# Kernel tuning notes

Hardware: AMD Instinct MI355X
Metric: run time of the kernel (lower is better)

The kernel has to match this reference:

```python
import jax, jax.numpy as jnp
import numpy as np

N0 = 50000  # nodes of type n0
N1 = 50000  # nodes of type n1
E = 160000  # edges per relation
IN_FEAT = 128
OUT_FEAT = 128
NUM_BASES = 2
NUM_RELS = 4


def setup_inputs() -> dict:
    key = jax.random.key(0)
    ks = jax.random.split(key, 12)
    inp = {
        "x0": jax.random.normal(ks[0], (N0, IN_FEAT), dtype=jnp.float32),
        "x1": jax.random.normal(ks[1], (N1, IN_FEAT), dtype=jnp.float32),
        "weight": jax.random.normal(ks[2], (NUM_BASES, IN_FEAT, OUT_FEAT), dtype=jnp.float32) * 0.05,
        "w_comp": jax.random.normal(ks[3], (NUM_RELS, NUM_BASES), dtype=jnp.float32),
        "h_bias": jnp.zeros((OUT_FEAT,), dtype=jnp.float32),
    }
    # relation i: (src ntype, dst ntype) = (0,0), (0,1), (1,0), (1,1)
    inp["src0"] = jax.random.randint(ks[4], (E,), 0, N0, dtype=jnp.int32)
    inp["dst0"] = jax.random.randint(ks[5], (E,), 0, N0, dtype=jnp.int32)
    inp["src1"] = jax.random.randint(ks[6], (E,), 0, N0, dtype=jnp.int32)
    inp["dst1"] = jax.random.randint(ks[7], (E,), 0, N1, dtype=jnp.int32)
    inp["src2"] = jax.random.randint(ks[8], (E,), 0, N1, dtype=jnp.int32)
    inp["dst2"] = jax.random.randint(ks[9], (E,), 0, N0, dtype=jnp.int32)
    inp["src3"] = jax.random.randint(ks[10], (E,), 0, N1, dtype=jnp.int32)
    inp["dst3"] = jax.random.randint(ks[11], (E,), 0, N1, dtype=jnp.int32)
    return inp


def _rel_msg(x_src, W_r, src, dst, n_dst):
    # per-relation: transform all src features, gather per edge, scatter-sum to dst
    h = x_src @ W_r            # [N_src, out]
    m = jnp.take(h, src, axis=0)  # [E, out]
    return jax.ops.segment_sum(m, dst, num_segments=n_dst)


def reference(x0, x1, weight, w_comp, h_bias,
              src0, dst0, src1, dst1, src2, dst2, src3, dst3):
    # basis regularizer: compose per-relation weights from shared bases
    W = jnp.einsum('rb,bio->rio', w_comp, weight)  # [num_rels, in, out]
    # cross-reducer 'sum': sum aggregated messages per destination node type
    agg0 = _rel_msg(x0, W[0], src0, dst0, N0) + _rel_msg(x1, W[2], src2, dst2, N0)
    agg1 = _rel_msg(x0, W[1], src1, dst1, N1) + _rel_msg(x1, W[3], src3, dst3, N1)
    h0 = agg0 + h_bias  # bias; activation=None, self_loop=False, dropout=0
    h1 = agg1 + h_bias
    return (h0, h1)
```

## Files before the change

### kernel.cpp

```cpp
#include <hip/hip_runtime.h>
#include <hip/hip_bf16.h>

typedef __bf16 bf16x8 __attribute__((ext_vector_type(8)));
typedef float f32x4 __attribute__((ext_vector_type(4)));

#define N_NODES 50000
#define NEDGE 160000
#define NSLOT (2 * N_NODES)
#define NB 3125
#define CAPS 96
#define SCAP 768
#define HSZ ((size_t)N_NODES * 128)
#define FILL_BLKS 2500
#define GEMM_BLKS 1564

constexpr size_t OFF_WFRAG = 0;
constexpr size_t OFF_H     = 131072;
constexpr size_t OFF_CNT   = OFF_H + 4 * 12800000;
constexpr size_t OFF_SBEG  = OFF_CNT + 1600000;
constexpr size_t OFF_SCNT  = OFF_SBEG + 401408;
constexpr size_t OFF_EBUF  = OFF_SCNT + 401408;
constexpr size_t OFF_SRC   = OFF_EBUF + 9600000;

__global__ __launch_bounds__(256) void wfrag_kernel(const float* __restrict__ weight,
                                                    const float* __restrict__ wcomp,
                                                    __bf16* __restrict__ wfrag,
                                                    int* __restrict__ cnt) {
    int tid = blockIdx.x * 256 + threadIdx.x;
    if (tid < NB * 8) cnt[tid * 16] = 0;
    int j    = tid & 7;
    int lane = (tid >> 3) & 63;
    int kk   = (tid >> 9) & 3;
    int n    = (tid >> 11) & 7;
    int r    = tid >> 14;
    int k = kk * 32 + ((lane >> 4) << 3) + j;
    int o = (n << 4) + (lane & 15);
    float v = wcomp[r * 2] * weight[k * 128 + o] +
              wcomp[r * 2 + 1] * weight[16384 + k * 128 + o];
    wfrag[tid] = (__bf16)v;
}

__global__ __launch_bounds__(256) void gemm_fill_kernel(const float* __restrict__ x0,
                                                        const float* __restrict__ x1,
                                                        const __bf16* __restrict__ wfrag,
                                                        __bf16* __restrict__ Hbase,
                                                        const int* __restrict__ s0, const int* __restrict__ d0,
                                                        const int* __restrict__ s1, const int* __restrict__ d1,
                                                        const int* __restrict__ s2, const int* __restrict__ d2,
                                                        const int* __restrict__ s3, const int* __restrict__ d3,
                                                        int* __restrict__ cnt,
                                                        unsigned int* __restrict__ ebuf) {
    __shared__ __bf16 wl[16384];
    int bid = blockIdx.x;

    if (bid < FILL_BLKS) {
        int rel = bid / 625;
        int e = (bid - rel * 625) * 256 + threadIdx.x;
        int sub = bid & 7;
        const int* sp = rel == 0 ? s0 : rel == 1 ? s1 : rel == 2 ? s2 : s3;
        const int* dp = rel == 0 ? d0 : rel == 1 ? d1 : rel == 2 ? d2 : d3;
        int slot = dp[e] + ((rel & 1) ? N_NODES : 0);
        unsigned int w = (unsigned)sp[e] | ((unsigned)(slot & 31) << 16) |
                         ((rel >= 2) ? (1u << 21) : 0u);
        int seg = (slot >> 5) * 8 + sub;
        int pos = atomicAdd(&cnt[seg * 16], 1);
        if (pos < CAPS) ebuf[seg * CAPS + pos] = w;
        return;
    }

    int gid = bid - FILL_BLKS;
    const int y = gid / 782;
    const int xb = gid - y * 782;
    const float* x = y ? x1 : x0;

    const int lane = threadIdx.x & 63;
    const int wave = threadIdx.x >> 6;
    const int g = lane >> 4;
    const int m15 = lane & 15;

    int node = xb * 64 + wave * 16 + m15;
    int rowc = node < N_NODES ? node : N_NODES - 1;
    const float* xr = x + (size_t)rowc * 128 + g * 8;

    bf16x8 a[4];
#pragma unroll
    for (int kk = 0; kk < 4; ++kk) {
        float4 f0 = *reinterpret_cast<const float4*>(xr + kk * 32);
        float4 f1 = *reinterpret_cast<const float4*>(xr + kk * 32 + 4);
        bf16x8 t;
        t[0] = (__bf16)f0.x; t[1] = (__bf16)f0.y; t[2] = (__bf16)f0.z; t[3] = (__bf16)f0.w;
        t[4] = (__bf16)f1.x; t[5] = (__bf16)f1.y; t[6] = (__bf16)f1.z; t[7] = (__bf16)f1.w;
        a[kk] = t;
    }

    const bf16x8* wv = reinterpret_cast<const bf16x8*>(wl);
    bool valid = node < N_NODES;

#pragma unroll
    for (int rr = 0; rr < 2; ++rr) {
        int rel = 2 * y + rr;
        if (rr) __syncthreads();
        {
            const uint4* s = reinterpret_cast<const uint4*>(wfrag + rel * 16384);
            uint4* dsl = reinterpret_cast<uint4*>(wl);
            int t = threadIdx.x;
#pragma unroll
            for (int i = 0; i < 8; ++i) dsl[t + i * 256] = s[t + i * 256];
        }
        __syncthreads();

        __bf16* H = Hbase + (size_t)rel * HSZ;
#pragma unroll
        for (int n = 0; n < 8; ++n) {
            f32x4 acc = (f32x4){0.f, 0.f, 0.f, 0.f};
#pragma unroll
            for (int kk = 0; kk < 4; ++kk)
                acc = __builtin_amdgcn_mfma_f32_16x16x32_bf16(
                    wv[(n * 4 + kk) * 64 + lane], a[kk], acc, 0, 0, 0);
            if (valid) {
                union { __bf16 b[4]; uint2 u; } pk;
                pk.b[0] = (__bf16)acc[0]; pk.b[1] = (__bf16)acc[1];
                pk.b[2] = (__bf16)acc[2]; pk.b[3] = (__bf16)acc[3];
                *reinterpret_cast<uint2*>(&H[(size_t)node * 128 + n * 16 + g * 4]) = pk.u;
            }
        }
    }
}

__global__ __launch_bounds__(256) void bucket_sort_kernel(const unsigned int* __restrict__ ebuf,
                                                          const int* __restrict__ cnt,
                                                          int* __restrict__ srcids,
                                                          int* __restrict__ sbeg,
                                                          unsigned int* __restrict__ scnt) {
    __shared__ int sbuf[SCAP];
    __shared__ int lcnt[64];
    __shared__ int lcur[64];
    __shared__ int stotal;
    int b = blockIdx.x;
    int t = threadIdx.x;
    if (t < 64) lcnt[t] = 0;
    for (int j = t; j < SCAP; j += 256) sbuf[j] = 0;
    __syncthreads();

    int cs[8];
#pragma unroll
    for (int s = 0; s < 8; ++s) {
        int c = cnt[(b * 8 + s) * 16];
        cs[s] = c < CAPS ? c : CAPS;
    }
#pragma unroll
    for (int s = 0; s < 8; ++s)
        for (int j = t; j < cs[s]; j += 256) {
            unsigned int w = ebuf[(b * 8 + s) * CAPS + j];
            int key = ((w >> 15) & 62) | ((w >> 21) & 1);
            atomicAdd(&lcnt[key], 1);
        }
    __syncthreads();

    if (t < 64) {
        int cA = (t < 32) ? lcnt[2 * t] : 0;
        int cB = (t < 32) ? lcnt[2 * t + 1] : 0;
        int pad = (cA + cB + 3) & ~3;
        int s = pad;
#pragma unroll
        for (int dd = 1; dd < 64; dd <<= 1) {
            int n = __shfl_up(s, dd, 64);
            if (t >= dd) s += n;
        }
        int start = s - pad;
        if (t < 32) {
            lcur[2 * t] = start;
            lcur[2 * t + 1] = start + cA;
            sbeg[b * 32 + t] = b * SCAP + start;
            scnt[b * 32 + t] = (unsigned)cA | ((unsigned)cB << 16);
            if (t == 31) stotal = start + pad;
        }
    }
    __syncthreads();

#pragma unroll
    for (int s = 0; s < 8; ++s)
        for (int j = t; j < cs[s]; j += 256) {
            unsigned int w = ebuf[(b * 8 + s) * CAPS + j];
            int key = ((w >> 15) & 62) | ((w >> 21) & 1);
            int pos = atomicAdd(&lcur[key], 1);
            sbuf[pos] = (int)(w & 0xffffu);
        }
    __syncthreads();

    int n = stotal;
    int* du = srcids + (size_t)b * SCAP;
    for (int j = t; j < n; j += 256) du[j] = sbuf[j];
}

__global__ __launch_bounds__(256) void aggregate_all_kernel(const __bf16* __restrict__ Hbase,
                                                            const int* __restrict__ sbeg,
                                                            const unsigned int* __restrict__ scnt,
                                                            const int* __restrict__ srcids,
                                                            const float* __restrict__ bias,
                                                            float* __restrict__ out) {
    int idx = blockIdx.x * 256 + threadIdx.x;
    int slot = idx >> 6;
    int lane = idx & 63;
    int p = slot >= N_NODES;

    int beg = __builtin_amdgcn_readfirstlane(sbeg[slot]);
    unsigned int c = (unsigned int)__builtin_amdgcn_readfirstlane((int)scnt[slot]);
    int dA = (int)(c & 0xffffu);
    int d  = dA + (int)(c >> 16);
    const int* sp = srcids + beg;

    const unsigned int* HA = reinterpret_cast<const unsigned int*>(Hbase + (size_t)p * HSZ);
    const unsigned int* HB = reinterpret_cast<const unsigned int*>(Hbase + (size_t)(p + 2) * HSZ);

    float2 bv = *reinterpret_cast<const float2*>(bias + 2 * lane);
    float acc0 = bv.x, acc1 = bv.y;

    for (int i = 0; i < d; i += 8) {
        int4 ca = *reinterpret_cast<const int4*>(sp + i);
        int4 cb = (d > i + 4) ? *reinterpret_cast<const int4*>(sp + i + 4) : ca;
        int ids[8] = {ca.x, ca.y, ca.z, ca.w, cb.x, cb.y, cb.z, cb.w};
        unsigned int hv[8];
#pragma unroll
        for (int k = 0; k < 8; ++k) {
            const unsigned int* Hp = (i + k < dA) ? HA : HB;
            unsigned int v = Hp[(size_t)(unsigned)ids[k] * 64 + lane];
            hv[k] = (i + k < d) ? v : 0u;
        }
#pragma unroll
        for (int k = 0; k < 8; ++k) {
            union { unsigned int u; float f; } lo, hi;
            lo.u = hv[k] << 16;
            hi.u = hv[k] & 0xFFFF0000u;
            acc0 += lo.f;
            acc1 += hi.f;
        }
    }
    *reinterpret_cast<float2*>(out + (size_t)slot * 128 + 2 * lane) =
        make_float2(acc0, acc1);
}

extern "C" void kernel_launch(void* const* d_in, const int* in_sizes, int n_in,
                              void* d_out, int out_size, void* d_ws, size_t ws_size,
                              hipStream_t stream) {
    const float* x0     = (const float*)d_in[0];
    const float* x1     = (const float*)d_in[1];
    const float* weight = (const float*)d_in[2];
    const float* wcomp  = (const float*)d_in[3];
    const float* bias   = (const float*)d_in[4];
    const int* src[4] = {(const int*)d_in[5], (const int*)d_in[7],
                         (const int*)d_in[9], (const int*)d_in[11]};
    const int* dst[4] = {(const int*)d_in[6], (const int*)d_in[8],
                         (const int*)d_in[10], (const int*)d_in[12]};
    float* out = (float*)d_out;

    char* ws = (char*)d_ws;
    __bf16* wfrag = (__bf16*)(ws + OFF_WFRAG);
    __bf16* Hbase = (__bf16*)(ws + OFF_H);
    int* cnt      = (int*)(ws + OFF_CNT);
    int* sbeg     = (int*)(ws + OFF_SBEG);
    unsigned int* scnt = (unsigned int*)(ws + OFF_SCNT);
    unsigned int* ebuf = (unsigned int*)(ws + OFF_EBUF);
    int* srcids   = (int*)(ws + OFF_SRC);

    wfrag_kernel<<<256, 256, 0, stream>>>(weight, wcomp, wfrag, cnt);

    gemm_fill_kernel<<<FILL_BLKS + GEMM_BLKS, 256, 0, stream>>>(
        x0, x1, wfrag, Hbase,
        src[0], dst[0], src[1], dst[1], src[2], dst[2], src[3], dst[3],
        cnt, ebuf);

    bucket_sort_kernel<<<NB, 256, 0, stream>>>(ebuf, cnt, srcids, sbeg, scnt);

    aggregate_all_kernel<<<NSLOT * 64 / 256, 256, 0, stream>>>(
        Hbase, sbeg, scnt, srcids, bias, out);
}
```

Measured before the change: 104.7 us.

## Fuse bucket sort into aggregation and interleave GEMM with fill blocks

Merges the bucket-sort and aggregation kernels so each block sorts its 32 destination slots into shared memory and then gathers and sums H rows directly from that shared buffer. This drops the global srcids/sbeg/scnt round trip and one kernel launch. Separately, GEMM and edge-fill blocks are now interleaved in the block index so compute-heavy and atomic-heavy work share the machine. The tradeoff is that aggregation parallelism drops to 4 waves per block each handling 8 slots serially, which may reduce latency hiding for the random gathers.

```diff
diff --git a/kernel.cpp b/kernel.cpp
--- a/kernel.cpp
+++ b/kernel.cpp
@@ -11,16 +11,14 @@
 #define CAPS 96
 #define SCAP 768
 #define HSZ ((size_t)N_NODES * 128)
+#define GEMM_BLKS 1564
 #define FILL_BLKS 2500
-#define GEMM_BLKS 1564
+#define TOTAL_BLKS (GEMM_BLKS + FILL_BLKS)
 
 constexpr size_t OFF_WFRAG = 0;
 constexpr size_t OFF_H     = 131072;
 constexpr size_t OFF_CNT   = OFF_H + 4 * 12800000;
-constexpr size_t OFF_SBEG  = OFF_CNT + 1600000;
-constexpr size_t OFF_SCNT  = OFF_SBEG + 401408;
-constexpr size_t OFF_EBUF  = OFF_SCNT + 401408;
-constexpr size_t OFF_SRC   = OFF_EBUF + 9600000;
+constexpr size_t OFF_EBUF  = OFF_CNT + 1600000;
 
 __global__ __launch_bounds__(256) void wfrag_kernel(const float* __restrict__ weight,
                                                     const float* __restrict__ wcomp,
@@ -53,9 +51,12 @@
     __shared__ __bf16 wl[16384];
     int bid = blockIdx.x;
 
-    if (bid < FILL_BLKS) {
-        int rel = bid / 625;
-        int e = (bid - rel * 625) * 256 + threadIdx.x;
+    bool is_gemm = (bid < 2 * GEMM_BLKS) && ((bid & 1) == 0);
+    if (!is_gemm) {
+        int fid = (bid < 2 * GEMM_BLKS) ? (bid >> 1)
+                                        : (GEMM_BLKS + (bid - 2 * GEMM_BLKS));
+        int rel = fid / 625;
+        int e = (fid - rel * 625) * 256 + threadIdx.x;
         int sub = bid & 7;
         const int* sp = rel == 0 ? s0 : rel == 1 ? s1 : rel == 2 ? s2 : s3;
         const int* dp = rel == 0 ? d0 : rel == 1 ? d1 : rel == 2 ? d2 : d3;
@@ -68,7 +69,7 @@
         return;
     }
 
-    int gid = bid - FILL_BLKS;
+    int gid = bid >> 1;
     const int y = gid / 782;
     const int xb = gid - y * 782;
     const float* x = y ? x1 : x0;
@@ -127,19 +128,18 @@
     }
 }
 
-__global__ __launch_bounds__(256) void bucket_sort_kernel(const unsigned int* __restrict__ ebuf,
-                                                          const int* __restrict__ cnt,
-                                                          int* __restrict__ srcids,
-                                                          int* __restrict__ sbeg,
-                                                          unsigned int* __restrict__ scnt) {
+__global__ __launch_bounds__(256) void sortagg_kernel(const unsigned int* __restrict__ ebuf,
+                                                      const int* __restrict__ cnt,
+                                                      const __bf16* __restrict__ Hbase,
+                                                      const float* __restrict__ bias,
+                                                      float* __restrict__ out) {
     __shared__ int sbuf[SCAP];
     __shared__ int lcnt[64];
+    __shared__ int lex[64];
     __shared__ int lcur[64];
-    __shared__ int stotal;
     int b = blockIdx.x;
     int t = threadIdx.x;
     if (t < 64) lcnt[t] = 0;
-    for (int j = t; j < SCAP; j += 256) sbuf[j] = 0;
     __syncthreads();
 
     int cs[8];
@@ -158,23 +158,15 @@
     __syncthreads();
 
     if (t < 64) {
-        int cA = (t < 32) ? lcnt[2 * t] : 0;
-        int cB = (t < 32) ? lcnt[2 * t + 1] : 0;
-        int pad = (cA + cB + 3) & ~3;
-        int s = pad;
+        int v = lcnt[t];
+        int s = v;
 #pragma unroll
         for (int dd = 1; dd < 64; dd <<= 1) {
             int n = __shfl_up(s, dd, 64);
             if (t >= dd) s += n;
         }
-        int start = s - pad;
-        if (t < 32) {
-            lcur[2 * t] = start;
-            lcur[2 * t + 1] = start + cA;
-            sbeg[b * 32 + t] = b * SCAP + start;
-            scnt[b * 32 + t] = (unsigned)cA | ((unsigned)cB << 16);
-            if (t == 31) stotal = start + pad;
-        }
+        lex[t] = s - v;
+        lcur[t] = s - v;
     }
     __syncthreads();
 
@@ -188,56 +180,49 @@
         }
     __syncthreads();
 
-    int n = stotal;
-    int* du = srcids + (size_t)b * SCAP;
-    for (int j = t; j < n; j += 256) du[j] = sbuf[j];
-}
-
-__global__ __launch_bounds__(256) void aggregate_all_kernel(const __bf16* __restrict__ Hbase,
-                                                            const int* __restrict__ sbeg,
-                                                            const unsigned int* __restrict__ scnt,
-                                                            const int* __restrict__ srcids,
-                                                            const float* __restrict__ bias,
-                                                            float* __restrict__ out) {
-    int idx = blockIdx.x * 256 + threadIdx.x;
-    int slot = idx >> 6;
-    int lane = idx & 63;
-    int p = slot >= N_NODES;
-
-    int beg = __builtin_amdgcn_readfirstlane(sbeg[slot]);
-    unsigned int c = (unsigned int)__builtin_amdgcn_readfirstlane((int)scnt[slot]);
-    int dA = (int)(c & 0xffffu);
-    int d  = dA + (int)(c >> 16);
-    const int* sp = srcids + beg;
-
-    const unsigned int* HA = reinterpret_cast<const unsigned int*>(Hbase + (size_t)p * HSZ);
-    const unsigned int* HB = reinterpret_cast<const unsigned int*>(Hbase + (size_t)(p + 2) * HSZ);
-
+    const int lane = t & 63;
+    const int wave = t >> 6;
+    const unsigned int* Hu = reinterpret_cast<const unsigned int*>(Hbase);
     float2 bv = *reinterpret_cast<const float2*>(bias + 2 * lane);
-    float acc0 = bv.x, acc1 = bv.y;
-
-    for (int i = 0; i < d; i += 8) {
-        int4 ca = *reinterpret_cast<const int4*>(sp + i);
-        int4 cb = (d > i + 4) ? *reinterpret_cast<const int4*>(sp + i + 4) : ca;
-        int ids[8] = {ca.x, ca.y, ca.z, ca.w, cb.x, cb.y, cb.z, cb.w};
-        unsigned int hv[8];
-#pragma unroll
-        for (int k = 0; k < 8; ++k) {
-            const unsigned int* Hp = (i + k < dA) ? HA : HB;
-            unsigned int v = Hp[(size_t)(unsigned)ids[k] * 64 + lane];
-            hv[k] = (i + k < d) ? v : 0u;
-        }
-#pragma unroll
-        for (int k = 0; k < 8; ++k) {
-            union { unsigned int u; float f; } lo, hi;
-            lo.u = hv[k] << 16;
-            hi.u = hv[k] & 0xFFFF0000u;
-            acc0 += lo.f;
-            acc1 += hi.f;
-        }
-    }
-    *reinterpret_cast<float2*>(out + (size_t)slot * 128 + 2 * lane) =
-        make_float2(acc0, acc1);
+
+    for (int q = 0; q < 8; ++q) {
+        int sl = wave * 8 + q;
+        int slot = b * 32 + sl;
+        int dA = lcnt[2 * sl];
+        int d  = dA + lcnt[2 * sl + 1];
+        int beg = lex[2 * sl];
+        int p = slot >= N_NODES;
+        const unsigned int* HA = Hu + (size_t)p * (HSZ / 2);
+        const unsigned int* HB = Hu + (size_t)(p + 2) * (HSZ / 2);
+
+        float acc0 = bv.x, acc1 = bv.y;
+        for (int i = 0; i < d; i += 8) {
+            int ids[8];
+            unsigned int hv[8];
+#pragma unroll
+            for (int k = 0; k < 8; ++k) {
+                int j = i + k;
+                int jc = j < d ? j : d - 1;
+                ids[k] = sbuf[beg + jc];
+            }
+#pragma unroll
+            for (int k = 0; k < 8; ++k) {
+                const unsigned int* Hp = (i + k < dA) ? HA : HB;
+                unsigned int v = Hp[(size_t)(unsigned)ids[k] * 64 + lane];
+                hv[k] = (i + k < d) ? v : 0u;
+            }
+#pragma unroll
+            for (int k = 0; k < 8; ++k) {
+                union { unsigned int u; float f; } lo, hi;
+                lo.u = hv[k] << 16;
+                hi.u = hv[k] & 0xFFFF0000u;
+                acc0 += lo.f;
+                acc1 += hi.f;
+            }
+        }
+        *reinterpret_cast<float2*>(out + (size_t)slot * 128 + 2 * lane) =
+            make_float2(acc0, acc1);
+    }
 }
 
 extern "C" void kernel_launch(void* const* d_in, const int* in_sizes, int n_in,
@@ -258,20 +243,14 @@
     __bf16* wfrag = (__bf16*)(ws + OFF_WFRAG);
     __bf16* Hbase = (__bf16*)(ws + OFF_H);
     int* cnt      = (int*)(ws + OFF_CNT);
-    int* sbeg     = (int*)(ws + OFF_SBEG);
-    unsigned int* scnt = (unsigned int*)(ws + OFF_SCNT);
     unsigned int* ebuf = (unsigned int*)(ws + OFF_EBUF);
-    int* srcids   = (int*)(ws + OFF_SRC);
 
     wfrag_kernel<<<256, 256, 0, stream>>>(weight, wcomp, wfrag, cnt);
 
-    gemm_fill_kernel<<<FILL_BLKS + GEMM_BLKS, 256, 0, stream>>>(
+    gemm_fill_kernel<<<TOTAL_BLKS, 256, 0, stream>>>(
         x0, x1, wfrag, Hbase,
         src[0], dst[0], src[1], dst[1], src[2], dst[2], src[3], dst[3],
         cnt, ebuf);
 
-    bucket_sort_kernel<<<NB, 256, 0, stream>>>(ebuf, cnt, srcids, sbeg, scnt);
-
-    aggregate_all_kernel<<<NSLOT * 64 / 256, 256, 0, stream>>>(
-        Hbase, sbeg, scnt, srcids, bias, out);
-}
+    sortagg_kernel<<<NB, 256, 0, stream>>>(ebuf, cnt, Hbase, bias, out);
+}
```

After: 95.83 us. 8.5% less time.
